# Performance work log

Hardware: AMD Instinct MI355X
Metric: run time of the kernel (lower is better)

Reference implementation:

```python
import jax, jax.numpy as jnp
import numpy as np

B, T, C, H = 2, 2048, 2048, 16
HD = C // H  # 128
WINDOW = 2048


def setup_inputs() -> dict:
    key = jax.random.key(0)
    k0, k1, k2 = jax.random.split(key, 3)
    s = 0.02  # GPT-2 style init scale
    return {
        "x": jax.random.normal(k0, (B, T, C), jnp.float32),
        "w_attn": jax.random.normal(k1, (3 * C, C), jnp.float32) * s,
        "b_attn": jnp.zeros((3 * C,), jnp.float32),
        "w_proj": jax.random.normal(k2, (C, C), jnp.float32) * s,
        "b_proj": jnp.zeros((C,), jnp.float32),
    }


def reference(x, w_attn, b_attn, w_proj, b_proj):
    Bb, Tt, Cc = x.shape
    # fused qkv projection (torch Linear: y = x @ W^T + b)
    qkv = x @ w_attn.T + b_attn                       # [B, T, 3C]
    q, k, v = jnp.split(qkv, 3, axis=2)

    def to_heads(t):
        return t.reshape(Bb, Tt, H, HD).transpose(0, 2, 1, 3)  # [B, H, T, HD]

    q, k, v = to_heads(q), to_heads(k), to_heads(v)
    K = k.shape[2]  # kv length (== T, no past_kv)

    attn = jnp.einsum('bhqd,bhkd->bhqk', q, k) / jnp.sqrt(jnp.float32(HD))
    # Faithful to source: mask[:, :, T-1:T, :K] — single tril row T-1 broadcast
    # over all query positions (for prefill K==T this row is all ones).
    mask_row = jnp.arange(K) <= (Tt - 1)              # [K] bool
    attn = jnp.where(mask_row[None, None, None, :], attn, -jnp.inf)
    weights = jax.nn.softmax(attn, axis=-1)            # [B, H, T, K]
    # dropout p=0.0 (eval): identity
    ctx = jnp.einsum('bhqk,bhkd->bhqd', weights, v)    # [B, H, T, HD]
    ctx = ctx.transpose(0, 2, 1, 3).reshape(Bb, Tt, Cc)
    out = ctx @ w_proj.T + b_proj                      # [B, T, C]
    return (out, k, v)  # (context, present_kv)
```

## Files before the change

### kernel.cpp

```cpp
#include <hip/hip_runtime.h>
#include <hip/hip_bf16.h>
#include <cstdint>
#include <cstddef>
#include <cmath>

typedef __attribute__((ext_vector_type(8))) short short8;
typedef __attribute__((ext_vector_type(4))) short bf16x4;
typedef __attribute__((ext_vector_type(4))) float f32x4;

static constexpr int BB = 2, T = 2048, C = 2048, H = 16, HD = 128;
static constexpr int M = BB * T;
static constexpr size_t BTC = (size_t)BB * T * C;

__device__ __forceinline__ short f2bf(float f) {
    union { float f; uint32_t u; } v; v.f = f;
    uint32_t u = v.u;
    uint32_t r = (u + 0x7fffu + ((u >> 16) & 1u)) >> 16;
    return (short)r;
}

__device__ __forceinline__ short f2bf_fast(float f) {
    __hip_bfloat16 h = __float2bfloat16(f);
    return *reinterpret_cast<short*>(&h);
}

__device__ __forceinline__ void gl_lds16(const void* g, void* l) {
    __builtin_amdgcn_global_load_lds(
        (const __attribute__((address_space(1))) unsigned int*)g,
        (__attribute__((address_space(3))) unsigned int*)l, 16, 0, 0);
}

__global__ void cvt_bf16(const float* __restrict__ in, short* __restrict__ out, int n) {
    int i = (blockIdx.x * 256 + threadIdx.x) * 8;
    if (i >= n) return;
    float4 a = *(const float4*)(in + i);
    float4 b = *(const float4*)(in + i + 4);
    short8 o;
    o[0] = f2bf(a.x); o[1] = f2bf(a.y); o[2] = f2bf(a.z); o[3] = f2bf(a.w);
    o[4] = f2bf(b.x); o[5] = f2bf(b.y); o[6] = f2bf(b.z); o[7] = f2bf(b.w);
    *(short8*)(out + i) = o;
}

__global__ void cvt_qkv_in(const float* __restrict__ x, const float* __restrict__ wa,
                           short* __restrict__ xb, short* __restrict__ wab) {
    int i = (blockIdx.x * 256 + threadIdx.x) * 8;
    const float* src;
    short* dst;
    if (i < (int)BTC) { src = x + i; dst = xb + i; }
    else { src = wa + (i - (int)BTC); dst = wab + (i - (int)BTC); }
    float4 a = *(const float4*)(src);
    float4 b = *(const float4*)(src + 4);
    short8 o;
    o[0] = f2bf(a.x); o[1] = f2bf(a.y); o[2] = f2bf(a.z); o[3] = f2bf(a.w);
    o[4] = f2bf(b.x); o[5] = f2bf(b.y); o[6] = f2bf(b.z); o[7] = f2bf(b.w);
    *(short8*)(dst) = o;
}

__launch_bounds__(512, 2)
__global__ void gemm_qkv256(const short* __restrict__ A, const short* __restrict__ Bw,
                            const float* __restrict__ bias, float* __restrict__ outF,
                            short* __restrict__ q_ws, short* __restrict__ k_ws) {
    extern __shared__ char lds[];
    constexpr int K = 2048, NKT = K / 64;
    constexpr int BUFSZ = 57344;

    int bid = blockIdx.x;
    int g = bid & 7, j = bid >> 3;
    int by = (g & 1) * 8 + (j >> 3);
    int bx = (g >> 1) * 8 + (j & 7);
    int row0 = by * 256, col0 = bx * 192;

    int t = threadIdx.x, w = t >> 6, l = t & 63;
    int lr = l & 15, lg = l >> 4;
    int wr = w >> 2, wc = w & 3;

    const char* Ab = (const char*)A;
    const char* Bb = (const char*)Bw;
    const char* srcb[7];
    int dstoff[7];
#pragma unroll
    for (int c = 0; c < 7; c++) {
        bool isA = c < 4;
        int coff = (isA ? c : c - 4) * 8192 + t * 16;
        int row = coff >> 7;
        int colb = (coff & 127) ^ ((row & 7) << 4);
        srcb[c] = isA ? Ab + (size_t)(row0 + row) * (K * 2) + colb
                      : Bb + (size_t)(col0 + row) * (K * 2) + colb;
        dstoff[c] = (isA ? 0 : 32768) + coff;
    }

    f32x4 acc[8][3] = {};

#pragma unroll
    for (int c = 0; c < 7; c++) gl_lds16(srcb[c], lds + dstoff[c]);
#pragma unroll
    for (int c = 0; c < 7; c++) gl_lds16(srcb[c] + 128, lds + BUFSZ + dstoff[c]);
    asm volatile("s_waitcnt vmcnt(7)" ::: "memory");
    __builtin_amdgcn_s_barrier();

    for (int kt = 0; kt < NKT; kt++) {
        const char* Abase = lds + (kt & 1) * BUFSZ;
        const char* Bbase = Abase + 32768;

        short8 bfr[3][2];
#pragma unroll
        for (int p = 0; p < 4; p++) {
            short8 af[2][2];
#pragma unroll
            for (int mi2 = 0; mi2 < 2; mi2++) {
                int row = wr * 128 + p * 32 + mi2 * 16 + lr;
#pragma unroll
                for (int ks = 0; ks < 2; ks++)
                    af[mi2][ks] = *(const short8*)(Abase + row * 128 +
                                  ((ks * 64 + lg * 16) ^ ((row & 7) << 4)));
            }
            if (p == 0) {
#pragma unroll
                for (int ni = 0; ni < 3; ni++) {
                    int row = wc * 48 + ni * 16 + lr;
#pragma unroll
                    for (int ks = 0; ks < 2; ks++)
                        bfr[ni][ks] = *(const short8*)(Bbase + row * 128 +
                                      ((ks * 64 + lg * 16) ^ ((row & 7) << 4)));
                }
            }
            __builtin_amdgcn_s_setprio(1);
#pragma unroll
            for (int ks = 0; ks < 2; ks++)
#pragma unroll
                for (int mi2 = 0; mi2 < 2; mi2++)
#pragma unroll
                    for (int ni = 0; ni < 3; ni++)
                        acc[p * 2 + mi2][ni] = __builtin_amdgcn_mfma_f32_16x16x32_bf16(
                            af[mi2][ks], bfr[ni][ks], acc[p * 2 + mi2][ni], 0, 0, 0);
            __builtin_amdgcn_s_setprio(0);
        }

        __builtin_amdgcn_s_barrier();
        if (kt + 2 < NKT) {
            int koff = (kt + 2) * 128;
            char* dbase = lds + (kt & 1) * BUFSZ;
#pragma unroll
            for (int c = 0; c < 7; c++) gl_lds16(srcb[c] + koff, dbase + dstoff[c]);
            asm volatile("s_waitcnt vmcnt(7)" ::: "memory");
        } else {
            asm volatile("s_waitcnt vmcnt(0)" ::: "memory");
        }
        __builtin_amdgcn_s_barrier();
    }

#pragma unroll
    for (int mi = 0; mi < 8; mi++) {
        int gr0 = row0 + wr * 128 + mi * 16 + lg * 4;
#pragma unroll
        for (int ni = 0; ni < 3; ni++) {
            int gc = col0 + wc * 48 + ni * 16 + lr;
            float bv = bias[gc];
            int sec = gc >> 11, cc = gc & 2047;
            int h = cc >> 7, d = cc & 127;
#pragma unroll
            for (int r = 0; r < 4; r++) {
                float val = acc[mi][ni][r] + bv;
                int gr = gr0 + r;
                int b = gr >> 11, tt = gr & 2047;
                size_t idx = ((size_t)(b * H + h) * T + tt) * HD + d;
                if (sec == 0) {
                    q_ws[idx] = f2bf(val);
                } else if (sec == 1) {
                    outF[BTC + idx] = val;
                    k_ws[idx] = f2bf(val);
                } else {
                    outF[2 * BTC + idx] = val;
                }
            }
        }
    }
}

template<int NI, int EPI, int NBX>
__launch_bounds__(512, 2)
__global__ void gemm8p(const short* __restrict__ A, const short* __restrict__ Bw,
                       const float* __restrict__ bias, float* __restrict__ outF,
                       int Ndim) {
    extern __shared__ char lds[];
    constexpr int K = 2048, NKT = K / 64;
    constexpr int NCH = 4 + NI;
    constexpr int BUFSZ = 32768 + NI * 8192;

    int bid = blockIdx.x;
    int nwg = gridDim.x;
    int swz = (bid & 7) * (nwg >> 3) + (bid >> 3);
    int by = swz / NBX, bx = swz % NBX;
    int row0 = by * 256, col0 = bx * (NI * 64);

    int t = threadIdx.x, w = t >> 6, l = t & 63;
    int lr = l & 15, lg = l >> 4;
    int wr = w >> 2, wc = w & 3;

    const char* srcb[NCH];
    int dstoff[NCH];
#pragma unroll
    for (int c = 0; c < NCH; c++) {
        bool isA = c < 4;
        int coff = (isA ? c : c - 4) * 8192 + t * 16;
        int row = coff >> 7;
        int colb = (coff & 127) ^ ((row & 7) << 4);
        srcb[c] = isA ? (const char*)A + (size_t)(row0 + row) * (K * 2) + colb
                      : (const char*)Bw + (size_t)(col0 + row) * (K * 2) + colb;
        dstoff[c] = (isA ? 0 : 32768) + coff;
    }

    f32x4 acc[8][NI] = {};

#pragma unroll
    for (int c = 0; c < NCH; c++) gl_lds16(srcb[c], lds + dstoff[c]);
#pragma unroll
    for (int c = 0; c < NCH; c++) gl_lds16(srcb[c] + 128, lds + BUFSZ + dstoff[c]);
    asm volatile("s_waitcnt vmcnt(%0)" :: "n"(NCH) : "memory");
    __builtin_amdgcn_s_barrier();

    for (int kt = 0; kt < NKT; kt++) {
        char* base = lds + (kt & 1) * BUFSZ;
        const char* Bbase = base + 32768;
        int koff = (kt + 2) * 128;
        bool pf = (kt + 2 < NKT);

        short8 bfr[NI][2];
#pragma unroll
        for (int p = 0; p < 4; p++) {
            short8 af[2][2];
#pragma unroll
            for (int mi2 = 0; mi2 < 2; mi2++) {
                int row = wr * 128 + p * 32 + mi2 * 16 + lr;
#pragma unroll
                for (int ks = 0; ks < 2; ks++)
                    af[mi2][ks] = *(const short8*)(base + row * 128 +
                                  ((ks * 64 + lg * 16) ^ ((row & 7) << 4)));
            }
            if (p == 0) {
#pragma unroll
                for (int ni = 0; ni < NI; ni++) {
                    int row = wc * (NI * 16) + ni * 16 + lr;
#pragma unroll
                    for (int ks = 0; ks < 2; ks++)
                        bfr[ni][ks] = *(const short8*)(Bbase + row * 128 +
                                      ((ks * 64 + lg * 16) ^ ((row & 7) << 4)));
                }
            }
            __builtin_amdgcn_s_barrier();
            __builtin_amdgcn_s_setprio(1);
#pragma unroll
            for (int ks = 0; ks < 2; ks++)
#pragma unroll
                for (int mi2 = 0; mi2 < 2; mi2++)
#pragma unroll
                    for (int ni = 0; ni < NI; ni++)
                        acc[p * 2 + mi2][ni] = __builtin_amdgcn_mfma_f32_16x16x32_bf16(
                            af[mi2][ks], bfr[ni][ks], acc[p * 2 + mi2][ni], 0, 0, 0);
            __builtin_amdgcn_s_setprio(0);
            __builtin_amdgcn_s_barrier();

            if (p == 0 && pf) {
#pragma unroll
                for (int c = 4; c < NCH; c++) gl_lds16(srcb[c] + koff, base + dstoff[c]);
            }
            if (p == 1 && pf) {
                gl_lds16(srcb[0] + koff, base + dstoff[0]);
                gl_lds16(srcb[2] + koff, base + dstoff[2]);
            }
            if (p == 3) {
                if (pf) {
                    gl_lds16(srcb[1] + koff, base + dstoff[1]);
                    gl_lds16(srcb[3] + koff, base + dstoff[3]);
                    asm volatile("s_waitcnt vmcnt(%0)" :: "n"(NCH) : "memory");
                } else {
                    asm volatile("s_waitcnt vmcnt(0)" ::: "memory");
                }
                __builtin_amdgcn_s_barrier();
            }
        }
    }

#pragma unroll
    for (int mi = 0; mi < 8; mi++) {
        int gr0 = row0 + wr * 128 + mi * 16 + lg * 4;
#pragma unroll
        for (int ni = 0; ni < NI; ni++) {
            int gc = col0 + wc * (NI * 16) + ni * 16 + lr;
            float bv = bias[gc];
#pragma unroll
            for (int r = 0; r < 4; r++)
                outF[(size_t)(gr0 + r) * Ndim + gc] = acc[mi][ni][r] + bv;
        }
    }
}

__global__ void vtrans(const float* __restrict__ vin, short* __restrict__ vT) {
    __shared__ float tile[64 * 65];
    int blk = blockIdx.x;
    int bh = blk >> 6, rem = blk & 63;
    int t0 = (rem >> 1) * 64, d0 = (rem & 1) * 64;
    const float* src = vin + (size_t)bh * T * HD;
    short* dst = vT + (size_t)bh * HD * T;
    int t = threadIdx.x;
#pragma unroll
    for (int i = 0; i < 16; i++) {
        int idx = i * 256 + t;
        int r = idx >> 6, c = idx & 63;
        tile[r * 65 + c] = src[(size_t)(t0 + r) * HD + d0 + c];
    }
    __syncthreads();
#pragma unroll
    for (int i = 0; i < 16; i++) {
        int idx = i * 256 + t;
        int rd = idx >> 6, cc = idx & 63;
        dst[(size_t)(d0 + rd) * T + t0 + cc] = f2bf(tile[cc * 65 + rd]);
    }
}

__launch_bounds__(256, 2)
__global__ void attn_fwd(const short* __restrict__ q_ws, const short* __restrict__ k_ws,
                         const short* __restrict__ vT_ws, short* __restrict__ ctx) {
    __shared__ __attribute__((aligned(16))) char K_lds[2][64 * 256];
    __shared__ __attribute__((aligned(16))) char VT_lds[2][128 * 128];
    __shared__ __attribute__((aligned(16))) char P_lds[4][16 * 128];

    int bid = blockIdx.x;
    int blk = (bid & 7) * 64 + (bid >> 3);
    int bh = blk >> 4;
    int q0 = (blk & 15) * 128;
    int b = bh >> 4, h = bh & 15;
    int t = threadIdx.x, w = t >> 6, l = t & 63;
    int lr = l & 15, lg = l >> 4;
    int sw = (lr & 7) << 4;

    short8 qf[2][4];
#pragma unroll
    for (int qt = 0; qt < 2; qt++) {
        const short* Qp = q_ws + ((size_t)bh * T + q0 + w * 32 + qt * 16 + lr) * HD;
#pragma unroll
        for (int c = 0; c < 4; c++) qf[qt][c] = *(const short8*)(Qp + c * 32 + lg * 8);
    }

    const char* Kp = (const char*)(k_ws + (size_t)bh * T * HD);
    const short* VTp = vT_ws + (size_t)bh * HD * T;
    char* Pc = P_lds[w];

    const float SC = 0.12753123813884803f;
    float m[2] = {-INFINITY, -INFINITY}, lsum[2] = {0.f, 0.f};
    f32x4 acc[2][8] = {};

    auto STAGE = [&](int kt, int bsel) {
#pragma unroll
        for (int i = 0; i < 4; i++) {
            int off = i * 4096 + t * 16;
            int swzK = off ^ (((off >> 8) & 7) << 4);
            gl_lds16(Kp + (size_t)kt * 16384 + swzK, K_lds[bsel] + off);
            int swzV = off ^ (((off >> 7) & 7) << 4);
            int row = swzV >> 7, cole = (swzV & 127) >> 1;
            gl_lds16(VTp + (size_t)row * T + kt * 64 + cole, VT_lds[bsel] + off);
        }
    };

    STAGE(0, 0);
    asm volatile("s_waitcnt vmcnt(0)" ::: "memory");
    __syncthreads();

    for (int kt = 0; kt < T / 64; kt++) {
        int cur = kt & 1;
        if (kt + 1 < T / 64) STAGE(kt + 1, cur ^ 1);
        const char* Kc = K_lds[cur];
        const char* Vc = VT_lds[cur];

        f32x4 sacc[2][4] = {};
#pragma unroll
        for (int kj = 0; kj < 4; kj++) {
            int rowb = (kj * 16 + lr) * 256;
#pragma unroll
            for (int c = 0; c < 4; c++) {
                short8 kf = *(const short8*)(Kc + ((rowb + c * 64 + lg * 16) ^ sw));
                sacc[0][kj] = __builtin_amdgcn_mfma_f32_16x16x32_bf16(kf, qf[0][c], sacc[0][kj], 0, 0, 0);
                sacc[1][kj] = __builtin_amdgcn_mfma_f32_16x16x32_bf16(kf, qf[1][c], sacc[1][kj], 0, 0, 0);
            }
        }

#pragma unroll
        for (int qt = 0; qt < 2; qt++) {
            float t0 = fmaxf(fmaxf(sacc[qt][0][0], sacc[qt][0][1]), fmaxf(sacc[qt][0][2], sacc[qt][0][3]));
            float t1 = fmaxf(fmaxf(sacc[qt][1][0], sacc[qt][1][1]), fmaxf(sacc[qt][1][2], sacc[qt][1][3]));
            float t2 = fmaxf(fmaxf(sacc[qt][2][0], sacc[qt][2][1]), fmaxf(sacc[qt][2][2], sacc[qt][2][3]));
            float t3 = fmaxf(fmaxf(sacc[qt][3][0], sacc[qt][3][1]), fmaxf(sacc[qt][3][2], sacc[qt][3][3]));
            float xm = fmaxf(fmaxf(t0, t1), fmaxf(t2, t3)) * SC;
            xm = fmaxf(xm, __shfl_xor(xm, 16));
            xm = fmaxf(xm, __shfl_xor(xm, 32));

            if (!__all(xm <= m[qt] + 8.0f)) {
                float mn = fmaxf(m[qt], xm);
                float al = __builtin_exp2f(m[qt] - mn);
                m[qt] = mn;
                lsum[qt] *= al;
                float ar[4];
#pragma unroll
                for (int r = 0; r < 4; r++) ar[r] = __shfl(al, lg * 4 + r);
#pragma unroll
                for (int nj = 0; nj < 8; nj++)
#pragma unroll
                    for (int r = 0; r < 4; r++) acc[qt][nj][r] *= ar[r];
            }

            float s0 = 0.f;
#pragma unroll
            for (int kj = 0; kj < 4; kj++) {
                bf16x4 pk;
#pragma unroll
                for (int r = 0; r < 4; r++) {
                    float pv = __builtin_exp2f(__builtin_fmaf(sacc[qt][kj][r], SC, -m[qt]));
                    s0 += pv;
                    pk[r] = f2bf_fast(pv);
                }
                *(bf16x4*)(Pc + ((lr * 128 + kj * 32 + lg * 8) ^ sw)) = pk;
            }
            s0 += __shfl_xor(s0, 16);
            s0 += __shfl_xor(s0, 32);
            lsum[qt] += s0;

            asm volatile("s_waitcnt lgkmcnt(0)" ::: "memory");

#pragma unroll
            for (int c2 = 0; c2 < 2; c2++) {
                short8 pf2 = *(const short8*)(Pc + ((lr * 128 + c2 * 64 + lg * 16) ^ sw));
#pragma unroll
                for (int nj = 0; nj < 8; nj++) {
                    short8 vf = *(const short8*)(Vc + (((nj * 16 + lr) * 128 + c2 * 64 + lg * 16) ^ sw));
                    acc[qt][nj] = __builtin_amdgcn_mfma_f32_16x16x32_bf16(pf2, vf, acc[qt][nj], 0, 0, 0);
                }
            }
        }

        asm volatile("s_waitcnt vmcnt(0)" ::: "memory");
        __syncthreads();
    }

#pragma unroll
    for (int qt = 0; qt < 2; qt++)
#pragma unroll
        for (int r = 0; r < 4; r++) {
            float rs = __shfl(lsum[qt], lg * 4 + r);
            float inv = 1.0f / rs;
            int tq = q0 + w * 32 + qt * 16 + lg * 4 + r;
            size_t base = ((size_t)b * T + tq) * C + h * HD;
#pragma unroll
            for (int nj = 0; nj < 8; nj++)
                ctx[base + nj * 16 + lr] = f2bf_fast(acc[qt][nj][r] * inv);
        }
}

extern "C" void kernel_launch(void* const* d_in, const int* in_sizes, int n_in,
                              void* d_out, int out_size, void* d_ws, size_t ws_size,
                              hipStream_t stream) {
    const float* x      = (const float*)d_in[0];
    const float* w_attn = (const float*)d_in[1];
    const float* b_attn = (const float*)d_in[2];
    const float* w_proj = (const float*)d_in[3];
    const float* b_proj = (const float*)d_in[4];
    float* out = (float*)d_out;

    char* ws = (char*)d_ws;
    short* x_bf  = (short*)ws;
    short* wp_bf = (short*)ws;
    short* wa_bf = (short*)(ws + 16777216);
    short* ctx   = (short*)(ws + 16777216);
    short* vT    = (short*)(ws + 41943040);

    short* q_ws = (short*)d_out;
    short* k_ws = (short*)d_out + BTC;

    hipFuncSetAttribute((const void*)gemm_qkv256,
                        hipFuncAttributeMaxDynamicSharedMemorySize, 114688);
    hipFuncSetAttribute((const void*)gemm8p<2, 1, 16>,
                        hipFuncAttributeMaxDynamicSharedMemorySize, 98304);

    cvt_qkv_in<<<10240, 256, 0, stream>>>(x, w_attn, x_bf, wa_bf);

    gemm_qkv256<<<512, 512, 114688, stream>>>(x_bf, wa_bf, b_attn, out, q_ws, k_ws);

    vtrans<<<2048, 256, 0, stream>>>(out + 2 * BTC, vT);
    cvt_bf16<<<2048, 256, 0, stream>>>(w_proj, wp_bf, C * C);

    attn_fwd<<<512, 256, 0, stream>>>(q_ws, k_ws, vT, ctx);

    gemm8p<2, 1, 16><<<256, 512, 98304, stream>>>(ctx, wp_bf, b_proj, out, 2048);
}
```

Measured before the change: 289.5 us.

## Restructure QKV GEMM main loop into 8-phase interleaved load/compute schedule

Rewrites the QKV projection GEMM main loop into an eight-phase-per-tile schedule. Each phase does a small slice of LDS fragment reads, issues a few global-to-LDS prefetch loads for the next tile, and runs a block of MFMAs between barriers. The goal is to spread memory traffic across the compute so that load latency and LDS reads overlap with MFMA work instead of bunching at tile boundaries. In exchange it adds many more barriers per tile, and the finer vmcnt bookkeeping is easy to get subtly wrong.

```diff
diff --git a/kernel.cpp b/kernel.cpp
--- a/kernel.cpp
+++ b/kernel.cpp
@@ -57,9 +57,9 @@
 }
 
 __launch_bounds__(512, 2)
-__global__ void gemm_qkv256(const short* __restrict__ A, const short* __restrict__ Bw,
-                            const float* __restrict__ bias, float* __restrict__ outF,
-                            short* __restrict__ q_ws, short* __restrict__ k_ws) {
+__global__ void gemm_qkv8p(const short* __restrict__ A, const short* __restrict__ Bw,
+                           const float* __restrict__ bias, float* __restrict__ outF,
+                           short* __restrict__ q_ws, short* __restrict__ k_ws) {
     extern __shared__ char lds[];
     constexpr int K = 2048, NKT = K / 64;
     constexpr int BUFSZ = 57344;
@@ -74,8 +74,6 @@
     int lr = l & 15, lg = l >> 4;
     int wr = w >> 2, wc = w & 3;
 
-    const char* Ab = (const char*)A;
-    const char* Bb = (const char*)Bw;
     const char* srcb[7];
     int dstoff[7];
 #pragma unroll
@@ -84,68 +82,105 @@
         int coff = (isA ? c : c - 4) * 8192 + t * 16;
         int row = coff >> 7;
         int colb = (coff & 127) ^ ((row & 7) << 4);
-        srcb[c] = isA ? Ab + (size_t)(row0 + row) * (K * 2) + colb
-                      : Bb + (size_t)(col0 + row) * (K * 2) + colb;
+        srcb[c] = isA ? (const char*)A + (size_t)(row0 + row) * (K * 2) + colb
+                      : (const char*)Bw + (size_t)(col0 + row) * (K * 2) + colb;
         dstoff[c] = (isA ? 0 : 32768) + coff;
     }
 
     f32x4 acc[8][3] = {};
 
-#pragma unroll
-    for (int c = 0; c < 7; c++) gl_lds16(srcb[c], lds + dstoff[c]);
-#pragma unroll
-    for (int c = 0; c < 7; c++) gl_lds16(srcb[c] + 128, lds + BUFSZ + dstoff[c]);
-    asm volatile("s_waitcnt vmcnt(7)" ::: "memory");
+    auto ST = [&](int c, int kt) {
+        gl_lds16(srcb[c] + kt * 128, lds + (kt & 1) * BUFSZ + dstoff[c]);
+    };
+    auto RD_A = [&](const char* Ab, int ks, int mih, short8* af) {
+#pragma unroll
+        for (int mi2 = 0; mi2 < 4; mi2++) {
+            int row = wr * 128 + mih * 64 + mi2 * 16 + lr;
+            af[mi2] = *(const short8*)(Ab + row * 128 +
+                       ((ks * 64 + lg * 16) ^ ((row & 7) << 4)));
+        }
+    };
+    auto RD_B = [&](const char* Bb, int ks, short8* bfr) {
+#pragma unroll
+        for (int ni = 0; ni < 3; ni++) {
+            int row = wc * 48 + ni * 16 + lr;
+            bfr[ni] = *(const short8*)(Bb + row * 128 +
+                       ((ks * 64 + lg * 16) ^ ((row & 7) << 4)));
+        }
+    };
+    auto MM = [&](short8* af, short8* bfr, int mih) {
+        __builtin_amdgcn_s_setprio(1);
+#pragma unroll
+        for (int mi2 = 0; mi2 < 4; mi2++)
+#pragma unroll
+            for (int ni = 0; ni < 3; ni++)
+                acc[mih * 4 + mi2][ni] = __builtin_amdgcn_mfma_f32_16x16x32_bf16(
+                    af[mi2], bfr[ni], acc[mih * 4 + mi2][ni], 0, 0, 0);
+        __builtin_amdgcn_s_setprio(0);
+    };
+
+#pragma unroll
+    for (int c = 0; c < 7; c++) ST(c, 0);
+    ST(0, 1); ST(2, 1);
+    asm volatile("s_waitcnt vmcnt(2)" ::: "memory");
     __builtin_amdgcn_s_barrier();
 
-    for (int kt = 0; kt < NKT; kt++) {
-        const char* Abase = lds + (kt & 1) * BUFSZ;
-        const char* Bbase = Abase + 32768;
-
-        short8 bfr[3][2];
-#pragma unroll
-        for (int p = 0; p < 4; p++) {
-            short8 af[2][2];
-#pragma unroll
-            for (int mi2 = 0; mi2 < 2; mi2++) {
-                int row = wr * 128 + p * 32 + mi2 * 16 + lr;
-#pragma unroll
-                for (int ks = 0; ks < 2; ks++)
-                    af[mi2][ks] = *(const short8*)(Abase + row * 128 +
-                                  ((ks * 64 + lg * 16) ^ ((row & 7) << 4)));
-            }
-            if (p == 0) {
-#pragma unroll
-                for (int ni = 0; ni < 3; ni++) {
-                    int row = wc * 48 + ni * 16 + lr;
-#pragma unroll
-                    for (int ks = 0; ks < 2; ks++)
-                        bfr[ni][ks] = *(const short8*)(Bbase + row * 128 +
-                                      ((ks * 64 + lg * 16) ^ ((row & 7) << 4)));
-                }
-            }
-            __builtin_amdgcn_s_setprio(1);
-#pragma unroll
-            for (int ks = 0; ks < 2; ks++)
-#pragma unroll
-                for (int mi2 = 0; mi2 < 2; mi2++)
-#pragma unroll
-                    for (int ni = 0; ni < 3; ni++)
-                        acc[p * 2 + mi2][ni] = __builtin_amdgcn_mfma_f32_16x16x32_bf16(
-                            af[mi2][ks], bfr[ni][ks], acc[p * 2 + mi2][ni], 0, 0, 0);
-            __builtin_amdgcn_s_setprio(0);
-        }
-
-        __builtin_amdgcn_s_barrier();
-        if (kt + 2 < NKT) {
-            int koff = (kt + 2) * 128;
-            char* dbase = lds + (kt & 1) * BUFSZ;
-#pragma unroll
-            for (int c = 0; c < 7; c++) gl_lds16(srcb[c] + koff, dbase + dstoff[c]);
-            asm volatile("s_waitcnt vmcnt(7)" ::: "memory");
+    for (int it = 0; it < NKT / 2; ++it) {
+        int ta = 2 * it, tb = ta + 1;
+        const char* A0 = lds;          const char* B0 = lds + 32768;
+        const char* A1 = lds + BUFSZ;  const char* B1 = lds + BUFSZ + 32768;
+        bool s2 = (ta + 2 < NKT), s3 = (tb + 2 < NKT);
+        short8 af[4], bfr[3];
+
+        RD_A(A0, 0, 0, af); RD_B(B0, 0, bfr);
+        ST(1, tb); ST(3, tb);
+        __builtin_amdgcn_s_barrier();
+        MM(af, bfr, 0);
+        __builtin_amdgcn_s_barrier();
+        RD_A(A0, 0, 1, af);
+        ST(4, tb); ST(5, tb);
+        __builtin_amdgcn_s_barrier();
+        MM(af, bfr, 1);
+        __builtin_amdgcn_s_barrier();
+        RD_A(A0, 1, 0, af); RD_B(B0, 1, bfr);
+        ST(6, tb);
+        __builtin_amdgcn_s_barrier();
+        MM(af, bfr, 0);
+        __builtin_amdgcn_s_barrier();
+        RD_A(A0, 1, 1, af);
+        if (s2) {
+            ST(0, ta + 2); ST(2, ta + 2);
+            asm volatile("s_waitcnt vmcnt(2)" ::: "memory");
         } else {
             asm volatile("s_waitcnt vmcnt(0)" ::: "memory");
         }
+        __builtin_amdgcn_s_barrier();
+        MM(af, bfr, 1);
+        __builtin_amdgcn_s_barrier();
+        RD_A(A1, 0, 0, af); RD_B(B1, 0, bfr);
+        if (s2) { ST(1, ta + 2); ST(3, ta + 2); }
+        __builtin_amdgcn_s_barrier();
+        MM(af, bfr, 0);
+        __builtin_amdgcn_s_barrier();
+        RD_A(A1, 0, 1, af);
+        if (s2) { ST(4, ta + 2); ST(5, ta + 2); }
+        __builtin_amdgcn_s_barrier();
+        MM(af, bfr, 1);
+        __builtin_amdgcn_s_barrier();
+        RD_A(A1, 1, 0, af); RD_B(B1, 1, bfr);
+        if (s2) ST(6, ta + 2);
+        __builtin_amdgcn_s_barrier();
+        MM(af, bfr, 0);
+        __builtin_amdgcn_s_barrier();
+        RD_A(A1, 1, 1, af);
+        if (s3) {
+            ST(0, tb + 2); ST(2, tb + 2);
+            asm volatile("s_waitcnt vmcnt(2)" ::: "memory");
+        } else {
+            asm volatile("s_waitcnt vmcnt(0)" ::: "memory");
+        }
+        __builtin_amdgcn_s_barrier();
+        MM(af, bfr, 1);
         __builtin_amdgcn_s_barrier();
     }
 
@@ -475,14 +510,14 @@
     short* q_ws = (short*)d_out;
     short* k_ws = (short*)d_out + BTC;
 
-    hipFuncSetAttribute((const void*)gemm_qkv256,
+    hipFuncSetAttribute((const void*)gemm_qkv8p,
                         hipFuncAttributeMaxDynamicSharedMemorySize, 114688);
     hipFuncSetAttribute((const void*)gemm8p<2, 1, 16>,
                         hipFuncAttributeMaxDynamicSharedMemorySize, 98304);
 
     cvt_qkv_in<<<10240, 256, 0, stream>>>(x, w_attn, x_bf, wa_bf);
 
-    gemm_qkv256<<<512, 512, 114688, stream>>>(x_bf, wa_bf, b_attn, out, q_ws, k_ws);
+    gemm_qkv8p<<<512, 512, 114688, stream>>>(x_bf, wa_bf, b_attn, out, q_ws, k_ws);
 
     vtrans<<<2048, 256, 0, stream>>>(out + 2 * BTC, vT);
     cvt_bf16<<<2048, 256, 0, stream>>>(w_proj, wp_bf, C * C);
```

New measurement: 286.2 us. About the same (-1.1%).
